# Kernel tuning notes

Measured on AMD Instinct MI355X. Metric: run time of the kernel, lower is better.

Reference implementation:

```python
import jax, jax.numpy as jnp
import numpy as np

B, T, D = 2, 2048, 2048
H, KV = 16, 4
HD = D // H            # 128
REP = H // KV          # 4 query heads per kv head


def setup_inputs() -> dict:
    key = jax.random.key(0)
    ks = jax.random.split(key, 5)
    scale = D ** -0.5
    x = jax.random.normal(ks[0], (B, T, D), dtype=jnp.float32)
    Wq = jax.random.normal(ks[1], (D, H * HD), dtype=jnp.float32) * scale
    Wk = jax.random.normal(ks[2], (D, KV * HD), dtype=jnp.float32) * scale
    Wv = jax.random.normal(ks[3], (D, KV * HD), dtype=jnp.float32) * scale
    Wo = jax.random.normal(ks[4], (H * HD, D), dtype=jnp.float32) * scale
    return {"x": x, "Wq": Wq, "Wk": Wk, "Wv": Wv, "Wo": Wo}


def reference(x, Wq, Wk, Wv, Wo):
    b, t, d = x.shape
    # projections; group query heads by their kv head (repeat_interleave order:
    # q head h uses kv head h // REP, i.e. heads are contiguous per group)
    q = (x @ Wq).reshape(b, t, KV, REP, HD)          # bt(g r)d -> b t g r d
    k = (x @ Wk).reshape(b, t, KV, HD)
    v = (x @ Wv).reshape(b, t, KV, HD)
    # scores: [B, KV, REP, T, T] -- equivalent to repeat_interleave of kv heads
    scores = jnp.einsum('btgrd,bsgd->bgrts', q, k) * (HD ** -0.5)
    causal = jnp.tril(jnp.ones((t, t), dtype=bool))
    scores = jnp.where(causal, scores, -jnp.inf)
    weights = jax.nn.softmax(scores, axis=-1)
    out = jnp.einsum('bgrts,bsgd->btgrd', weights, v).reshape(b, t, H * HD)
    return jnp.round(out @ Wo, decimals=4)
```

## Files before the change

kernel.cpp:

```cpp
#include <hip/hip_runtime.h>
#include <hip/hip_bf16.h>
#include <math.h>

#define B_ 2
#define T_ 2048
#define D_ 2048
#define H_ 16
#define KV_ 4
#define HD_ 128
#define REP_ 4
#define QKVSTR 3072

typedef __attribute__((ext_vector_type(8))) short s16x8;
typedef __attribute__((ext_vector_type(4))) short s16x4;
typedef __attribute__((ext_vector_type(4))) float f32x4;
typedef __attribute__((ext_vector_type(16))) float f32x16;
typedef __hip_bfloat16 bf16;

__device__ __forceinline__ short f2bf(float x) {
    bf16 h = __float2bfloat16(x);
    return *reinterpret_cast<short*>(&h);
}

__device__ __forceinline__ void gl2lds16(const void* g, void* l) {
    __builtin_amdgcn_global_load_lds(
        (const __attribute__((address_space(1))) char*)g,
        (__attribute__((address_space(3))) char*)l, 16, 0, 0);
}

__global__ __launch_bounds__(256) void prep(const float* __restrict__ x,
                                            const float* __restrict__ Wq,
                                            const float* __restrict__ Wk,
                                            const float* __restrict__ Wv,
                                            const float* __restrict__ Wo,
                                            bf16* __restrict__ xb,
                                            bf16* __restrict__ Wqkvt,
                                            bf16* __restrict__ Wot,
                                            float qscale) {
    const int bid = blockIdx.x;
    const int t = threadIdx.x;
    if (bid < 4096) {
        int i = (bid * 256 + t) * 8;
        float4 a = *(const float4*)(x + i);
        float4 b = *(const float4*)(x + i + 4);
        short o[8] = {f2bf(a.x), f2bf(a.y), f2bf(a.z), f2bf(a.w),
                      f2bf(b.x), f2bf(b.y), f2bf(b.z), f2bf(b.w)};
        *(s16x8*)(xb + i) = *(const s16x8*)o;
        return;
    }
    __shared__ short tile[64 * 72];
    const float* W; bf16* dst; int N; float scale; int seg;
    if (bid < 5120)      { seg = bid - 4096; W = Wq; dst = Wqkvt;                      N = 2048; scale = qscale; }
    else if (bid < 5376) { seg = bid - 5120; W = Wk; dst = Wqkvt + (size_t)2048 * D_;  N = 512;  scale = 1.f; }
    else if (bid < 5632) { seg = bid - 5376; W = Wv; dst = Wqkvt + (size_t)2560 * D_;  N = 512;  scale = 1.f; }
    else                 { seg = bid - 5632; W = Wo; dst = Wot;                        N = 2048; scale = 1.f; }
    const int k0 = (seg & 31) * 64, n0 = (seg >> 5) * 64;
    const int r = t >> 2, c0 = (t & 3) * 16;
    const float* src = W + (size_t)(k0 + r) * N + n0 + c0;
    #pragma unroll
    for (int i = 0; i < 16; i += 4) {
        float4 v = *(const float4*)(src + i);
        tile[r * 72 + c0 + i + 0] = f2bf(v.x * scale);
        tile[r * 72 + c0 + i + 1] = f2bf(v.y * scale);
        tile[r * 72 + c0 + i + 2] = f2bf(v.z * scale);
        tile[r * 72 + c0 + i + 3] = f2bf(v.w * scale);
    }
    __syncthreads();
    short tmp[16];
    #pragma unroll
    for (int i = 0; i < 16; ++i) tmp[i] = tile[(c0 + i) * 72 + r];
    bf16* d = dst + (size_t)(n0 + r) * D_ + k0 + c0;
    *(s16x8*)(d)     = *(const s16x8*)&tmp[0];
    *(s16x8*)(d + 8) = *(const s16x8*)&tmp[8];
}

template<typename OUTT, int ROUND, int WVT>
__global__ __launch_bounds__(256, 3) void gemm_nt(const bf16* __restrict__ A,
                                                  const bf16* __restrict__ Bt,
                                                  OUTT* __restrict__ C,
                                                  bf16* __restrict__ Vtg,
                                                  int M, int N, int K) {
    __shared__ short As[128 * 64];
    __shared__ short Bs[128 * 64];
    const int tid = threadIdx.x;
    const int lane = tid & 63;
    const int wave = tid >> 6;
    const int quad = lane >> 4;
    const int l16 = lane & 15;
    const int wr = wave >> 1, wc = wave & 1;
    const int row0 = blockIdx.y * 128;
    const int col0 = blockIdx.x * 128;

    f32x4 acc[4][4] = {};

    for (int k0 = 0; k0 < K; k0 += 64) {
        __syncthreads();
        #pragma unroll
        for (int i = 0; i < 4; ++i) {
            int g = i * 256 + tid;
            int row = g >> 3;
            int cs = (g & 7) ^ (row & 7);
            gl2lds16(A + (size_t)(row0 + row) * K + k0 + cs * 8, &As[g * 8]);
        }
        #pragma unroll
        for (int i = 0; i < 4; ++i) {
            int g = i * 256 + tid;
            int row = g >> 3;
            int cs = (g & 7) ^ (row & 7);
            gl2lds16(Bt + (size_t)(col0 + row) * K + k0 + cs * 8, &Bs[g * 8]);
        }
        __syncthreads();
        #pragma unroll
        for (int kk = 0; kk < 2; ++kk) {
            s16x8 af[4], bfr[4];
            #pragma unroll
            for (int i = 0; i < 4; ++i) {
                int row = wr * 64 + i * 16 + l16;
                int c = (kk * 4 + quad) ^ (row & 7);
                af[i] = *(const s16x8*)&As[row * 64 + c * 8];
            }
            #pragma unroll
            for (int j = 0; j < 4; ++j) {
                int row = wc * 64 + j * 16 + l16;
                int c = (kk * 4 + quad) ^ (row & 7);
                bfr[j] = *(const s16x8*)&Bs[row * 64 + c * 8];
            }
            #pragma unroll
            for (int i = 0; i < 4; ++i)
                #pragma unroll
                for (int j = 0; j < 4; ++j)
                    acc[i][j] = __builtin_amdgcn_mfma_f32_16x16x32_bf16(
                        af[i], bfr[j], acc[i][j], 0, 0, 0);
        }
    }

    #pragma unroll
    for (int i = 0; i < 4; ++i) {
        #pragma unroll
        for (int j = 0; j < 4; ++j) {
            const int col = col0 + wc * 64 + j * 16 + l16;
            const int rowb = row0 + wr * 64 + i * 16 + quad * 4;
            #pragma unroll
            for (int r = 0; r < 4; ++r) {
                float v = acc[i][j][r];
                if (ROUND) v = rintf(v * 1e4f) * 1e-4f;
                if constexpr (sizeof(OUTT) == 2)
                    C[(size_t)(rowb + r) * N + col] = __float2bfloat16(v);
                else
                    C[(size_t)(rowb + r) * N + col] = v;
            }
            if constexpr (WVT) {
                if (col >= 2560) {
                    const int dcol = (col - 2560) & 127;
                    const int g = (col - 2560) >> 7;
                    const int b = rowb >> 11;
                    const int t = rowb & 2047;
                    short pk[4] = {f2bf(acc[i][j][0]), f2bf(acc[i][j][1]),
                                   f2bf(acc[i][j][2]), f2bf(acc[i][j][3])};
                    *(s16x4*)&Vtg[(size_t)((b * KV_ + g) * HD_ + dcol) * T_ + t] =
                        *(const s16x4*)pk;
                }
            }
        }
    }
}

__global__ __launch_bounds__(256, 3) void flash8(const bf16* __restrict__ Q,
                                                 const bf16* __restrict__ K,
                                                 const bf16* __restrict__ Vtg,
                                                 bf16* __restrict__ O) {
    __shared__ short smem[16384];

    const int h = blockIdx.x;
    const int b = blockIdx.y & 1;
    const int qt = 15 - (blockIdx.y >> 1);
    const int g = h >> 2;
    const int tid = threadIdx.x;
    const int lane = tid & 63;
    const int wave = tid >> 6;
    const int l32 = lane & 31;
    const int hi = lane >> 5;
    const int qw0 = qt * 128 + wave * 32;
    const int qg = qw0 + l32;

    s16x8 qf[8];
    {
        const bf16* qp = Q + (size_t)(b * T_ + qg) * QKVSTR + h * HD_ + hi * 8;
        #pragma unroll
        for (int kt = 0; kt < 8; ++kt) qf[kt] = *(const s16x8*)(qp + kt * 16);
    }

    const bf16* Kp = K + (size_t)(b * T_) * QKVSTR + g * HD_;
    const bf16* Vp = Vtg + (size_t)((b * KV_ + g) * HD_) * T_;

    float l_part = 0.f;
    f32x16 oacc[4] = {};

    const int jmax = 2 * qt + 1;
    for (int j = 0; j <= jmax; ++j) {
        const int s0 = j * 64;
        __syncthreads();
        #pragma unroll
        for (int i = 0; i < 4; ++i) {
            int g2 = i * 256 + tid;
            int s = g2 >> 4;
            int cs = (g2 & 15) ^ (s & 15);
            gl2lds16(Kp + (size_t)(s0 + s) * QKVSTR + cs * 8, &smem[g2 * 8]);
        }
        #pragma unroll
        for (int i = 0; i < 4; ++i) {
            int g2 = i * 256 + tid;
            int d = g2 >> 3;
            int cs = (g2 & 7) ^ (d & 7);
            gl2lds16(Vp + (size_t)d * T_ + s0 + cs * 8, &smem[8192 + g2 * 8]);
        }
        __syncthreads();

        if (s0 >= qw0 + 32) continue;

        f32x16 sacc[2] = {};
        #pragma unroll
        for (int kt = 0; kt < 8; ++kt) {
            #pragma unroll
            for (int mt = 0; mt < 2; ++mt) {
                int s = mt * 32 + l32;
                int c = (kt * 2 + hi) ^ (s & 15);
                const s16x8 kf = *(const s16x8*)&smem[s * 128 + c * 8];
                sacc[mt] = __builtin_amdgcn_mfma_f32_32x32x16_bf16(
                    kf, qf[kt], sacc[mt], 0, 0, 0);
            }
        }

        const bool diagw = (s0 + 63 > qw0);
        #pragma unroll
        for (int mt = 0; mt < 2; ++mt) {
            #pragma unroll
            for (int r = 0; r < 16; ++r) {
                float sv = sacc[mt][r];
                if (diagw) {
                    int sg = s0 + mt * 32 + (r & 3) + 8 * (r >> 2) + 4 * hi;
                    if (sg > qg) sv = -INFINITY;
                }
                float e = exp2f(sv);
                sacc[mt][r] = e;
                l_part += e;
            }
            #pragma unroll
            for (int kts = 0; kts < 2; ++kts) {
                const int o = kts * 8;
                unsigned w01, w23, w45, w67;
                asm("v_cvt_pk_bf16_f32 %0, %1, %2"
                    : "=v"(w01) : "v"(sacc[mt][o + 0]), "v"(sacc[mt][o + 1]));
                asm("v_cvt_pk_bf16_f32 %0, %1, %2"
                    : "=v"(w23) : "v"(sacc[mt][o + 2]), "v"(sacc[mt][o + 3]));
                asm("v_cvt_pk_bf16_f32 %0, %1, %2"
                    : "=v"(w45) : "v"(sacc[mt][o + 4]), "v"(sacc[mt][o + 5]));
                asm("v_cvt_pk_bf16_f32 %0, %1, %2"
                    : "=v"(w67) : "v"(sacc[mt][o + 6]), "v"(sacc[mt][o + 7]));
                asm("v_permlane32_swap_b32 %0, %1" : "+v"(w01), "+v"(w45));
                asm("v_permlane32_swap_b32 %0, %1" : "+v"(w23), "+v"(w67));
                union { unsigned u[4]; s16x8 v; } pu;
                pu.u[0] = w01; pu.u[1] = w23; pu.u[2] = w45; pu.u[3] = w67;
                const s16x8 pa = pu.v;
                #pragma unroll
                for (int nt = 0; nt < 4; ++nt) {
                    int d = nt * 32 + l32;
                    int c = ((mt * 2 + kts) * 2 + hi) ^ (d & 7);
                    const s16x8 vf = *(const s16x8*)&smem[8192 + d * 64 + c * 8];
                    oacc[nt] = __builtin_amdgcn_mfma_f32_32x32x16_bf16(
                        pa, vf, oacc[nt], 0, 0, 0);
                }
            }
        }
    }

    l_part += __shfl_xor(l_part, 32);
    const float invl = 1.f / l_part;

    bf16* op = O + (size_t)(b * T_ + qw0) * (H_ * HD_) + h * HD_;
    #pragma unroll
    for (int r = 0; r < 16; ++r) {
        const int qrow = (r & 3) + 8 * (r >> 2) + 4 * hi;
        const float il = __shfl(invl, qrow);
        #pragma unroll
        for (int nt = 0; nt < 4; ++nt)
            op[(size_t)qrow * (H_ * HD_) + nt * 32 + l32] =
                __float2bfloat16(oacc[nt][r] * il);
    }
}

extern "C" void kernel_launch(void* const* d_in, const int* in_sizes, int n_in,
                              void* d_out, int out_size, void* d_ws, size_t ws_size,
                              hipStream_t stream) {
    const float* x  = (const float*)d_in[0];
    const float* Wq = (const float*)d_in[1];
    const float* Wk = (const float*)d_in[2];
    const float* Wv = (const float*)d_in[3];
    const float* Wo = (const float*)d_in[4];
    float* out = (float*)d_out;

    const size_t NR = (size_t)B_ * T_;
    bf16* ws = (bf16*)d_ws;
    bf16* xb    = ws;
    bf16* Wqkvt = xb + NR * D_;
    bf16* Wot   = Wqkvt + (size_t)QKVSTR * D_;
    bf16* QKVb  = Wot + (size_t)D_ * D_;
    bf16* Vtg   = QKVb + NR * QKVSTR;
    bf16* Ab    = Vtg + (size_t)B_ * KV_ * HD_ * T_;

    const float qscale = 1.4426950408889634f / sqrtf((float)HD_);

    prep<<<6656, 256, 0, stream>>>(x, Wq, Wk, Wv, Wo, xb, Wqkvt, Wot, qscale);

    gemm_nt<bf16, 0, 1><<<dim3(QKVSTR / 128, NR / 128), 256, 0, stream>>>(
        xb, Wqkvt, QKVb, Vtg, (int)NR, QKVSTR, D_);

    flash8<<<dim3(H_, 32), 256, 0, stream>>>(QKVb, QKVb + 2048, Vtg, Ab);

    gemm_nt<float, 1, 0><<<dim3(D_ / 128, NR / 128), 256, 0, stream>>>(
        Ab, Wot, out, nullptr, (int)NR, D_, H_ * HD_);
}
```

Measured before the change: 325.2 us.

## Double-buffer K/V tiles in LDS to prefetch the next block during compute

The flash attention kernel now keeps two LDS buffers for K and V tiles. It issues the global-to-LDS loads for tile j+1 before computing on tile j, and a prologue loads the first tile. This removes one barrier per iteration and is meant to hide the latency of loading K/V behind the MFMA and softmax work. In exchange, LDS use per block doubles to 64 KB and the launch bound drops from 3 to 2 blocks per CU, which lowers occupancy.

```diff
diff --git a/kernel.cpp b/kernel.cpp
--- a/kernel.cpp
+++ b/kernel.cpp
@@ -165,11 +165,11 @@
     }
 }
 
-__global__ __launch_bounds__(256, 3) void flash8(const bf16* __restrict__ Q,
+__global__ __launch_bounds__(256, 2) void flash9(const bf16* __restrict__ Q,
                                                  const bf16* __restrict__ K,
                                                  const bf16* __restrict__ Vtg,
                                                  bf16* __restrict__ O) {
-    __shared__ short smem[16384];
+    __shared__ short smem[32768];
 
     const int h = blockIdx.x;
     const int b = blockIdx.y & 1;
@@ -197,25 +197,46 @@
     f32x16 oacc[4] = {};
 
     const int jmax = 2 * qt + 1;
+
+    #pragma unroll
+    for (int i = 0; i < 4; ++i) {
+        int g2 = i * 256 + tid;
+        int s = g2 >> 4;
+        int cs = (g2 & 15) ^ (s & 15);
+        gl2lds16(Kp + (size_t)s * QKVSTR + cs * 8, &smem[g2 * 8]);
+    }
+    #pragma unroll
+    for (int i = 0; i < 4; ++i) {
+        int g2 = i * 256 + tid;
+        int d = g2 >> 3;
+        int cs = (g2 & 7) ^ (d & 7);
+        gl2lds16(Vp + (size_t)d * T_ + cs * 8, &smem[8192 + g2 * 8]);
+    }
+
     for (int j = 0; j <= jmax; ++j) {
+        const int kb = (j & 1) << 14;
+        __syncthreads();
+
+        if (j < jmax) {
+            const int s0n = (j + 1) * 64;
+            const int nb = ((j + 1) & 1) << 14;
+            #pragma unroll
+            for (int i = 0; i < 4; ++i) {
+                int g2 = i * 256 + tid;
+                int s = g2 >> 4;
+                int cs = (g2 & 15) ^ (s & 15);
+                gl2lds16(Kp + (size_t)(s0n + s) * QKVSTR + cs * 8, &smem[nb + g2 * 8]);
+            }
+            #pragma unroll
+            for (int i = 0; i < 4; ++i) {
+                int g2 = i * 256 + tid;
+                int d = g2 >> 3;
+                int cs = (g2 & 7) ^ (d & 7);
+                gl2lds16(Vp + (size_t)d * T_ + s0n + cs * 8, &smem[nb + 8192 + g2 * 8]);
+            }
+        }
+
         const int s0 = j * 64;
-        __syncthreads();
-        #pragma unroll
-        for (int i = 0; i < 4; ++i) {
-            int g2 = i * 256 + tid;
-            int s = g2 >> 4;
-            int cs = (g2 & 15) ^ (s & 15);
-            gl2lds16(Kp + (size_t)(s0 + s) * QKVSTR + cs * 8, &smem[g2 * 8]);
-        }
-        #pragma unroll
-        for (int i = 0; i < 4; ++i) {
-            int g2 = i * 256 + tid;
-            int d = g2 >> 3;
-            int cs = (g2 & 7) ^ (d & 7);
-            gl2lds16(Vp + (size_t)d * T_ + s0 + cs * 8, &smem[8192 + g2 * 8]);
-        }
-        __syncthreads();
-
         if (s0 >= qw0 + 32) continue;
 
         f32x16 sacc[2] = {};
@@ -225,7 +246,7 @@
             for (int mt = 0; mt < 2; ++mt) {
                 int s = mt * 32 + l32;
                 int c = (kt * 2 + hi) ^ (s & 15);
-                const s16x8 kf = *(const s16x8*)&smem[s * 128 + c * 8];
+                const s16x8 kf = *(const s16x8*)&smem[kb + s * 128 + c * 8];
                 sacc[mt] = __builtin_amdgcn_mfma_f32_32x32x16_bf16(
                     kf, qf[kt], sacc[mt], 0, 0, 0);
             }
@@ -266,7 +287,7 @@
                 for (int nt = 0; nt < 4; ++nt) {
                     int d = nt * 32 + l32;
                     int c = ((mt * 2 + kts) * 2 + hi) ^ (d & 7);
-                    const s16x8 vf = *(const s16x8*)&smem[8192 + d * 64 + c * 8];
+                    const s16x8 vf = *(const s16x8*)&smem[kb + 8192 + d * 64 + c * 8];
                     oacc[nt] = __builtin_amdgcn_mfma_f32_32x32x16_bf16(
                         pa, vf, oacc[nt], 0, 0, 0);
                 }
@@ -315,7 +336,7 @@
     gemm_nt<bf16, 0, 1><<<dim3(QKVSTR / 128, NR / 128), 256, 0, stream>>>(
         xb, Wqkvt, QKVb, Vtg, (int)NR, QKVSTR, D_);
 
-    flash8<<<dim3(H_, 32), 256, 0, stream>>>(QKVb, QKVb + 2048, Vtg, Ab);
+    flash9<<<dim3(H_, 32), 256, 0, stream>>>(QKVb, QKVb + 2048, Vtg, Ab);
 
     gemm_nt<float, 1, 0><<<dim3(D_ / 128, NR / 128), 256, 0, stream>>>(
         Ab, Wot, out, nullptr, (int)NR, D_, H_ * HD_);
```

New measurement: 276.4 us. -15.0%, faster.
